# Performance work log

Measured on AMD Instinct MI355X. Metric: run time of the kernel, lower is better.

Reference implementation:

```python
import jax, jax.numpy as jnp
import numpy as np

EPS = 1e-7
BURN_IN = 3
INNER_STEPS = 2
N_FEAT, N_TARGET, N_LATENT = 262144, 8192, 32


def setup_inputs() -> dict:
    key = jax.random.key(0)
    ks = jax.random.split(key, 8)
    x = jax.random.normal(ks[0], (N_FEAT,), jnp.float32)
    y = jax.random.normal(ks[1], (N_TARGET,), jnp.float32)
    mu_x = jnp.zeros((N_FEAT,), jnp.float32)
    mu_y = jnp.zeros((N_TARGET,), jnp.float32)
    u0 = jax.random.normal(ks[2], (N_LATENT,), jnp.float32)
    u = u0 / jnp.sqrt(jnp.sum(u0 ** 2))
    Wz = jax.random.normal(ks[3], (N_LATENT, N_FEAT), jnp.float32) * 0.1
    Cz = jax.random.normal(ks[4], (N_LATENT, N_TARGET), jnp.float32) * 0.1
    t_sq_sum = jax.random.uniform(ks[5], (N_LATENT,), jnp.float32) + 1.0
    bz = jax.random.normal(ks[6], (N_LATENT,), jnp.float32) * 0.1
    P = jax.random.normal(ks[7], (N_LATENT, N_FEAT), jnp.float32) * 0.1
    return dict(x=x, y=y, mu_x=mu_x, mu_y=mu_y, u=u, Wz=Wz, Cz=Cz,
                t_sq_sum=t_sq_sum, bz=bz, P=P, n=100)


def _partial_fit(x, y, mu_x, mu_y, u, Wz, Cz, t_sq_sum, bz, P, n):
    # n is a static Python int (sample count before this call)
    n_new = n + 1  # torch: self.n[:] = self.n + 1
    mu_x = (mu_x * n_new + x) / (n_new + 1)
    mu_y = (mu_y * n_new + y) / (n_new + 1)
    xc = x - mu_x
    yc = y - mu_y
    if n_new <= BURN_IN:
        # vectorized burn-in update; only Wz and t_sq_sum change
        Wz = Wz + xc[None, :] * u[:, None]
        tz = Wz @ xc / (jnp.sqrt(jnp.sum(Wz ** 2, axis=1)) + EPS)
        t_sq_sum = t_sq_sum + tz * tz
        return mu_x, mu_y, u, Wz, Cz, t_sq_sum, bz, P

    def comp_step(carry, comp):
        xr, yr = carry
        Wz_i, Cz_i, P_i, u_i, tss, bz_i = comp
        # inner power-iteration refinements (total INNER_STEPS passes)
        for _ in range(INNER_STEPS):
            wz = Wz_i + xr * u_i                                  # [n_feat]
            tz = xr @ wz / (jnp.sqrt(jnp.sum(wz ** 2)) + EPS)     # scalar
            tss_ = tss + tz * tz
            t = tz / jnp.sqrt(tss_)
            cz = Cz_i + yr * t                                    # [n_target]
            C_i = cz / jnp.sqrt(jnp.sum(cz ** 2))
            u_i = yr @ C_i
        bz_new = bz_i + u_i * tz
        b = bz_new / jnp.sqrt(tss_)
        P_new = P_i + xr * t
        xr2 = xr - t * P_new  # deflate x
        yr2 = yr - b * t * C_i  # deflate y
        return (xr2, yr2), (wz, cz, P_new, u_i, tss_, bz_new)

    (_, _), (Wz_n, Cz_n, P_n, u_n, tss_n, bz_n) = jax.lax.scan(
        comp_step, (xc, yc), (Wz, Cz, P, u, t_sq_sum, bz))
    return mu_x, mu_y, u_n, Wz_n, Cz_n, tss_n, bz_n, P_n


def reference(x, y, mu_x, mu_y, u, Wz, Cz, t_sq_sum, bz, P, n):
    outs = _partial_fit(x, y, mu_x, mu_y, u, Wz, Cz, t_sq_sum, bz, P, n)
    # concatenate updated state (mu_x, mu_y, u, Wz, Cz, t_sq_sum, bz, P)
    return jnp.concatenate([o.ravel() for o in outs])
```

## Files before the change

kernel.cpp:

```cpp
#include <hip/hip_runtime.h>


#define NF 262144
#define NT 8192
#define NL 32
#define GYS 36
#define LDSW 260

#define NBX 1024
#define KS  256
#define CHK 128
#define NSLOT 512
#define GXW 68
#define PBE 2276
#define DIAG 2244

#define WS_PART 0
#define WS_GY   (NSLOT*PBE)
#define WS_GX   (WS_GY + GYS*GYS)
#define WS_CNT  (WS_GX + PBE)
#define WS_COEF (WS_CNT + 4)

#define OUT_MU_X 0
#define OUT_MU_Y 262144
#define OUT_U    270336
#define OUT_WZ   270368
#define OUT_CZ   8658976
#define OUT_TSS  8921120
#define OUT_BZ   8921152
#define OUT_P    8921184

typedef __attribute__((ext_vector_type(8))) short bf16x8;
typedef __attribute__((ext_vector_type(4))) float f32x4;

__device__ __forceinline__ float4 ld4(const float* p) { return *(const float4*)p; }

__device__ __forceinline__ unsigned int f2bf_rne(float f) {
  unsigned int t = __float_as_uint(f);
  t += 0x7FFFu + ((t >> 16) & 1u);
  return t >> 16;
}

__device__ __forceinline__ double rsq64(double x) {
  double r = __builtin_amdgcn_rsq(x);
  r = r * (1.5 - 0.5 * x * r * r);
  return r;
}

__global__ __launch_bounds__(320) void gram_kernel(
    const float* __restrict__ x, const float* __restrict__ y,
    const float* __restrict__ mux, const float* __restrict__ muy,
    const float* __restrict__ Wz, const float* __restrict__ Cz,
    const float* __restrict__ P, const int* __restrict__ np,
    float* __restrict__ ws)
{
  __shared__ __align__(16) char smem[80 * CHK * 4 + 128];
  const int tid = threadIdx.x;
  const int b = blockIdx.x;
  const float n1 = (float)(np[0] + 1);
  const float cmu = n1 / (n1 + 1.0f);

  if (b < NBX) {
    char* hB = smem;
    char* lB = smem + 80 * CHK * 2;
    float* PB = ws + WS_PART + (size_t)(b & (NSLOT - 1)) * PBE;

    {
      unsigned int* hz = (unsigned int*)hB;
      unsigned int* lz = (unsigned int*)lB;
      for (int i = tid; i < 960; i += 320) { hz[65 * 64 + i] = 0u; lz[65 * 64 + i] = 0u; }
    }

    f32x4 acc0 = {0.f, 0.f, 0.f, 0.f};
    f32x4 acc1 = acc0, acc2 = acc0;
    const int lane = tid & 63;
    const int w = tid >> 6;
    const int col16 = lane & 15;
    const int kgrp = lane >> 4;
    const int swz = (col16 & 7) << 4;

    float4 v[7]; float4 vm0;

    auto issue = [&](int c) {
      const int kb = b * KS + c * CHK;
#pragma unroll
      for (int it = 0; it < 7; ++it) {
        int idx = tid + it * 320;
        if (idx < 2080) {
          int row = idx >> 5;
          int c4 = idx & 31;
          int k = kb + c4 * 4;
          const float* bp = (row == 0) ? (x + k)
                          : (row < 33) ? (P + (size_t)(row - 1) * NF + k)
                                       : (Wz + (size_t)(row - 33) * NF + k);
          v[it] = ld4(bp);
          if (it == 0 && row == 0) vm0 = ld4(mux + k);
        }
      }
    };

    auto convert_write = [&]() {
#pragma unroll
      for (int it = 0; it < 7; ++it) {
        int idx = tid + it * 320;
        if (idx < 2080) {
          int row = idx >> 5;
          int c4 = idx & 31;
          float4 t4 = v[it];
          if (it == 0 && row == 0) {
            t4.x = cmu * (t4.x - vm0.x); t4.y = cmu * (t4.y - vm0.y);
            t4.z = cmu * (t4.z - vm0.z); t4.w = cmu * (t4.w - vm0.w);
          }
          if (row >= 33) {
            float sq = t4.x * t4.x + t4.y * t4.y + t4.z * t4.z + t4.w * t4.w;
            sq += __shfl_xor(sq, 1, 64);
            sq += __shfl_xor(sq, 2, 64);
            sq += __shfl_xor(sq, 4, 64);
            sq += __shfl_xor(sq, 8, 64);
            sq += __shfl_xor(sq, 16, 64);
            if ((tid & 31) == 0) atomicAdd(&PB[DIAG + row - 33], sq);
          }
          unsigned int b0 = __float_as_uint(t4.x), b1 = __float_as_uint(t4.y);
          unsigned int b2 = __float_as_uint(t4.z), b3 = __float_as_uint(t4.w);
          float h0 = __uint_as_float(b0 & 0xFFFF0000u);
          float h1 = __uint_as_float(b1 & 0xFFFF0000u);
          float h2 = __uint_as_float(b2 & 0xFFFF0000u);
          float h3 = __uint_as_float(b3 & 0xFFFF0000u);
          uint2 hw, lw;
          hw.x = (b0 >> 16) | ((b1 >> 16) << 16);
          hw.y = (b2 >> 16) | ((b3 >> 16) << 16);
          lw.x = f2bf_rne(t4.x - h0) | (f2bf_rne(t4.y - h1) << 16);
          lw.y = f2bf_rne(t4.z - h2) | (f2bf_rne(t4.w - h3) << 16);
          int off = ((row << 8) + (c4 << 3)) ^ ((row & 7) << 4);
          *(uint2*)(hB + off) = hw;
          *(uint2*)(lB + off) = lw;
        }
      }
    };

    auto compute_chunk = [&]() {
#pragma unroll
      for (int s = 0; s < 4; ++s) {
        const int kbyte = s * 64 + kgrp * 16;
        const int oa = ((col16 << 8) + kbyte) ^ swz;
        const int ob = oa + (w << 12);
        bf16x8 bh = *(const bf16x8*)(hB + ob);
        bf16x8 bl = *(const bf16x8*)(lB + ob);
        bf16x8 a0h = *(const bf16x8*)(hB + oa);
        bf16x8 a0l = *(const bf16x8*)(lB + oa);
        acc0 = __builtin_amdgcn_mfma_f32_16x16x32_bf16(a0h, bh, acc0, 0, 0, 0);
        acc0 = __builtin_amdgcn_mfma_f32_16x16x32_bf16(a0h, bl, acc0, 0, 0, 0);
        acc0 = __builtin_amdgcn_mfma_f32_16x16x32_bf16(a0l, bh, acc0, 0, 0, 0);
        acc0 = __builtin_amdgcn_mfma_f32_16x16x32_bf16(a0l, bl, acc0, 0, 0, 0);
        bf16x8 a1h = *(const bf16x8*)(hB + oa + 4096);
        bf16x8 a1l = *(const bf16x8*)(lB + oa + 4096);
        acc1 = __builtin_amdgcn_mfma_f32_16x16x32_bf16(a1h, bh, acc1, 0, 0, 0);
        acc1 = __builtin_amdgcn_mfma_f32_16x16x32_bf16(a1h, bl, acc1, 0, 0, 0);
        acc1 = __builtin_amdgcn_mfma_f32_16x16x32_bf16(a1l, bh, acc1, 0, 0, 0);
        acc1 = __builtin_amdgcn_mfma_f32_16x16x32_bf16(a1l, bl, acc1, 0, 0, 0);
        bf16x8 a2h = *(const bf16x8*)(hB + oa + 8192);
        bf16x8 a2l = *(const bf16x8*)(lB + oa + 8192);
        acc2 = __builtin_amdgcn_mfma_f32_16x16x32_bf16(a2h, bh, acc2, 0, 0, 0);
        acc2 = __builtin_amdgcn_mfma_f32_16x16x32_bf16(a2h, bl, acc2, 0, 0, 0);
        acc2 = __builtin_amdgcn_mfma_f32_16x16x32_bf16(a2l, bh, acc2, 0, 0, 0);
        acc2 = __builtin_amdgcn_mfma_f32_16x16x32_bf16(a2l, bl, acc2, 0, 0, 0);
      }
    };

    issue(0);
    convert_write();
    __syncthreads();
    issue(1);
    compute_chunk();
    __syncthreads();
    convert_write();
    __syncthreads();
    compute_chunk();

    const int vcol = w * 16 + col16;
    if (vcol < 65) {
#pragma unroll
      for (int r2 = 0; r2 < 4; ++r2) {
        int u = kgrp * 4 + r2;
        atomicAdd(&PB[u * GXW + vcol], acc0[r2]);
        atomicAdd(&PB[(16 + u) * GXW + vcol], acc1[r2]);
      }
      if (kgrp == 0) atomicAdd(&PB[32 * GXW + vcol], acc2[0]);
    }
  } else {
    float* lds = (float*)smem;
    float* GY = ws + WS_GY;
    const int yb = b - NBX;
    int gu = 0, gv = 0; bool active = (tid < 45);
    if (active) {
      int pp = tid;
      for (int g = 0; g < 9; ++g) {
        int cnt = 9 - g;
        if (pp < cnt) { gu = g; gv = g + pp; break; }
        pp -= cnt;
      }
    }
    float acc[16];
#pragma unroll
    for (int i = 0; i < 16; ++i) acc[i] = 0.f;
    const int wb = yb * 256;
    float4 vy[8]; float4 vmy;
#pragma unroll
    for (int it = 0; it < 8; ++it) {
      int idx = tid + it * 320;
      if (idx < 2304) {
        int row = idx >> 6;
        int c4 = idx & 63;
        int k = wb + c4 * 4;
        if (row == 0) {
          vy[it] = ld4(y + k);
          if (it == 0) vmy = ld4(muy + k);
        } else if (row < 33) {
          vy[it] = ld4(Cz + (size_t)(row - 1) * NT + k);
        } else {
          vy[it] = make_float4(0.f, 0.f, 0.f, 0.f);
        }
      }
    }
#pragma unroll
    for (int it = 0; it < 8; ++it) {
      int idx = tid + it * 320;
      if (idx < 2304) {
        int row = idx >> 6;
        int c4 = idx & 63;
        float4 t4 = vy[it];
        if (it == 0 && row == 0) {
          t4.x = cmu * (t4.x - vmy.x); t4.y = cmu * (t4.y - vmy.y);
          t4.z = cmu * (t4.z - vmy.z); t4.w = cmu * (t4.w - vmy.w);
        }
        *(float4*)&lds[row * LDSW + c4 * 4] = t4;
      }
    }
    __syncthreads();
    if (active) {
      const int ub = 4 * gu * LDSW, vb = 4 * gv * LDSW;
      for (int c = 0; c < 64; ++c) {
        float4 av[4], bv[4];
#pragma unroll
        for (int r = 0; r < 4; ++r) av[r] = *(const float4*)&lds[ub + r * LDSW + c * 4];
#pragma unroll
        for (int s = 0; s < 4; ++s) bv[s] = *(const float4*)&lds[vb + s * LDSW + c * 4];
#pragma unroll
        for (int r = 0; r < 4; ++r)
#pragma unroll
          for (int s = 0; s < 4; ++s)
            acc[r * 4 + s] += av[r].x * bv[s].x + av[r].y * bv[s].y +
                              av[r].z * bv[s].z + av[r].w * bv[s].w;
      }
#pragma unroll
      for (int r = 0; r < 4; ++r)
#pragma unroll
        for (int s = 0; s < 4; ++s) {
          int u = 4 * gu + r, v = 4 * gv + s;
          if (u < 33 && v < 33) {
            float val = acc[r * 4 + s];
            atomicAdd(&GY[u * GYS + v], val);
            if (gu != gv) atomicAdd(&GY[v * GYS + u], val);
          }
        }
    }
  }
}

__device__ __forceinline__ void solve_body(
    const float* __restrict__ ws, const float* __restrict__ u_in,
    const float* __restrict__ tss_in, const float* __restrict__ bz_in,
    float* __restrict__ coef, float* __restrict__ out)
{
  const int l = threadIdx.x;
  const float* GX = ws + WS_GX;
  const float* GY = ws + WS_GY;
  float* AWZT = coef;
  float* APT  = coef + 33 * NL;
  float* ACZT = coef + 66 * NL;

  float rP[32], rW[32], rC[32];
#pragma unroll
  for (int i = 0; i < 32; ++i) rP[i] = GX[(1 + i) * GXW + 1 + l];
#pragma unroll
  for (int i = 0; i < 32; ++i) rW[i] = (l < 32) ? GX[(1 + i) * GXW + 33 + l] : 0.f;
#pragma unroll
  for (int i = 0; i < 32; ++i) rC[i] = GY[(1 + i) * GYS + 1 + l];
  float dS  = (l < 32) ? GX[DIAG + l] : 0.f;
  float u0l = (l < 32) ? u_in[l]   : 0.f;
  float t0l = (l < 32) ? tss_in[l] : 0.f;
  float b0l = (l < 32) ? bz_in[l]  : 0.f;

  double q = (double)GX[0];
  double r = (double)GY[0];
  double pj = (l < 32) ? (double)GX[1 + l]  : 0.0;
  double wj = (l < 32) ? (double)GX[33 + l] : 0.0;
  double ej = (l < 32) ? (double)GY[1 + l]  : 0.0;
  double cx = (l == 0) ? 1.0 : 0.0;
  double cy = (l == 0) ? 1.0 : 0.0;

#pragma unroll
  for (int i = 0; i < NL; ++i) {
    double a  = __shfl(wj, i, 64);
    double g  = __shfl(ej, i, 64);
    double pi = __shfl(pj, i, 64);
    double s  = (double)__shfl(dS, i, 64);
    double h  = (double)__shfl(rC[i], i, 64);
    double Pd = (double)__shfl(rP[i], i, 64);
    double u0   = (double)__shfl(u0l, i, 64);
    double tss0 = (double)__shfl(t0l, i, 64);
    double bz0  = (double)__shfl(b0l, i, 64);

    double ui = u0, u1 = 0.0, tz = 0.0, tss_ = 0.0, t = 0.0;
    double rt = 0.0, rn = 0.0;
#pragma unroll
    for (int pass = 0; pass < 2; ++pass) {
      double num = a + ui * q;
      double s2  = s + 2.0 * ui * a + ui * ui * q;
      double rs  = rsq64(s2);
      tz = num * rs * (1.0 - 1e-7 * rs);
      tss_ = tss0 + tz * tz;
      rt = rsq64(tss_);
      t  = tz * rt;
      double ncz2 = h + 2.0 * t * g + t * t * r;
      rn = rsq64(ncz2);
      ui = (g + t * r) * rn;
      if (pass == 0) u1 = ui;
    }
    double u2 = ui;
    double bz_new = bz0 + u2 * tz;
    double bb = bz_new * rt;
    double phi = 1.0 - t * t;
    double gam = bb * t * rn;
    double psi = 1.0 - gam * t;

    if (l == 0) {
      out[OUT_U + i]   = (float)u2;
      out[OUT_TSS + i] = (float)tss_;
      out[OUT_BZ + i]  = (float)bz_new;
    }
    if (l < 33) {
      AWZT[l * 32 + i] = (float)(u1 * cx);
      APT [l * 32 + i] = (float)(t  * cx) + ((l == 1 + i) ? 1.0f : 0.0f);
      ACZT[l * 32 + i] = (float)(t  * cy) + ((l == 1 + i) ? 1.0f : 0.0f);
    }
    q = phi * phi * q - 2.0 * phi * t * pi + t * t * Pd;
    r = psi * psi * r - 2.0 * psi * gam * g + gam * gam * h;
    cx *= phi; if (l == 1 + i) cx -= t;
    cy *= psi; if (l == 1 + i) cy -= gam;
    if (l < 32) {
      pj = phi * pj - t * (double)rP[i];
      wj = phi * wj - t * (double)rW[i];
      ej = psi * ej - gam * (double)rC[i];
    }
  }
}

__global__ __launch_bounds__(256) void redsolve_kernel(
    float* __restrict__ ws, const float* __restrict__ u_in,
    const float* __restrict__ tss_in, const float* __restrict__ bz_in,
    float* __restrict__ coef, float* __restrict__ out)
{
  const int e = (blockIdx.x % 9) * 256 + threadIdx.x;
  const int c = blockIdx.x / 9;
  if (e < PBE) {
    const float* PB = ws + WS_PART + (size_t)(c * 64) * PBE + e;
    float s0 = 0.f, s1 = 0.f, s2 = 0.f, s3 = 0.f;
#pragma unroll
    for (int j = 0; j < 64; j += 4) {
      s0 += PB[(size_t)j * PBE];
      s1 += PB[(size_t)(j + 1) * PBE];
      s2 += PB[(size_t)(j + 2) * PBE];
      s3 += PB[(size_t)(j + 3) * PBE];
    }
    atomicAdd(ws + WS_GX + e, (s0 + s1) + (s2 + s3));
  }
  __threadfence();
  __shared__ int lastflag;
  if (threadIdx.x == 0) {
    int old = atomicAdd((int*)(ws + WS_CNT), 1);
    lastflag = (old == 71);
  }
  __syncthreads();
  if (!lastflag) return;
  __threadfence();
  if (threadIdx.x < 64) solve_body(ws, u_in, tss_in, bz_in, coef, out);
}

__global__ __launch_bounds__(256) void out_kernel(
    const float* __restrict__ x, const float* __restrict__ y,
    const float* __restrict__ mux, const float* __restrict__ muy,
    const float* __restrict__ Wz, const float* __restrict__ Cz,
    const float* __restrict__ P, const int* __restrict__ np,
    const float* __restrict__ coef, float* __restrict__ out)
{
  const int b = blockIdx.x, tid = threadIdx.x;
  const float n1 = (float)(np[0] + 1);
  const float inv = 1.0f / (n1 + 1.0f);
  const float* AWZT = coef;
  const float* APT  = coef + 33 * NL;
  const float* ACZT = coef + 66 * NL;

  if (b < 1024) {
    const int k = b * 256 + tid;
    float xv = x[k], mv = mux[k];
    float mn = (mv * n1 + xv) * inv;
    out[OUT_MU_X + k] = mn;
    float accW[32], accP[32];
#pragma unroll
    for (int i = 0; i < 32; ++i) accW[i] = Wz[(size_t)i * NF + k];
#pragma unroll
    for (int i = 0; i < 32; ++i) accP[i] = 0.f;
    {
      float B0 = xv - mn;
#pragma unroll
      for (int i = 0; i < 32; ++i) {
        accW[i] += AWZT[i] * B0;
        accP[i] += APT[i] * B0;
      }
    }
#pragma unroll 4
    for (int j = 1; j < 33; ++j) {
      float Bj = P[(size_t)(j - 1) * NF + k];
      const float* cw = AWZT + j * 32;
      const float* cp = APT + j * 32;
#pragma unroll
      for (int i = 0; i < 32; ++i) {
        accW[i] += cw[i] * Bj;
        accP[i] += cp[i] * Bj;
      }
    }
#pragma unroll
    for (int i = 0; i < 32; ++i) out[OUT_WZ + (size_t)i * NF + k] = accW[i];
#pragma unroll
    for (int i = 0; i < 32; ++i) out[OUT_P + (size_t)i * NF + k] = accP[i];
  } else {
    const int k = (b - 1024) * 256 + tid;
    float yv = y[k], mv = muy[k];
    float mn = (mv * n1 + yv) * inv;
    out[OUT_MU_Y + k] = mn;
    float accC[32];
#pragma unroll
    for (int i = 0; i < 32; ++i) accC[i] = 0.f;
    {
      float B0 = yv - mn;
#pragma unroll
      for (int i = 0; i < 32; ++i) accC[i] += ACZT[i] * B0;
    }
#pragma unroll 4
    for (int j = 1; j < 33; ++j) {
      float Bj = Cz[(size_t)(j - 1) * NT + k];
      const float* cc = ACZT + j * 32;
#pragma unroll
      for (int i = 0; i < 32; ++i) accC[i] += cc[i] * Bj;
    }
#pragma unroll
    for (int i = 0; i < 32; ++i) out[OUT_CZ + (size_t)i * NT + k] = accC[i];
  }
}

extern "C" void kernel_launch(void* const* d_in, const int* in_sizes, int n_in,
                              void* d_out, int out_size, void* d_ws, size_t ws_size,
                              hipStream_t stream) {
  const float* x   = (const float*)d_in[0];
  const float* y   = (const float*)d_in[1];
  const float* mux = (const float*)d_in[2];
  const float* muy = (const float*)d_in[3];
  const float* u   = (const float*)d_in[4];
  const float* Wz  = (const float*)d_in[5];
  const float* Cz  = (const float*)d_in[6];
  const float* tss = (const float*)d_in[7];
  const float* bz  = (const float*)d_in[8];
  const float* P   = (const float*)d_in[9];
  const int*   n   = (const int*)d_in[10];
  float* ws  = (float*)d_ws;
  float* out = (float*)d_out;

  hipMemsetAsync(ws, 0, (size_t)(NSLOT * PBE + GYS * GYS + PBE + 4) * sizeof(float), stream);
  gram_kernel<<<NBX + 32, 320, 0, stream>>>(x, y, mux, muy, Wz, Cz, P, n, ws);
  redsolve_kernel<<<72, 256, 0, stream>>>(ws, u, tss, bz, ws + WS_COEF, out);
  out_kernel<<<1024 + 32, 256, 0, stream>>>(x, y, mux, muy, Wz, Cz, P, n, ws + WS_COEF, out);
}
```

Before: 220.4 us.

## Give each Gram block its own partial slot and loop over eight smaller chunks

Measured after the change: 208.7 us. -5.3%, faster.

```diff
diff --git a/kernel.cpp b/kernel.cpp
--- a/kernel.cpp
+++ b/kernel.cpp
@@ -5,18 +5,19 @@
 #define NT 8192
 #define NL 32
 #define GYS 36
-#define LDSW 260
-
-#define NBX 1024
-#define KS  256
-#define CHK 128
-#define NSLOT 512
+#define LDSWY 132
+
+#define NBX 512
+#define NBY 64
+#define KS  512
+#define CHK 64
+#define NCHK 8
 #define GXW 68
 #define PBE 2276
 #define DIAG 2244
 
 #define WS_PART 0
-#define WS_GY   (NSLOT*PBE)
+#define WS_GY   (NBX*PBE)
 #define WS_GX   (WS_GY + GYS*GYS)
 #define WS_CNT  (WS_GX + PBE)
 #define WS_COEF (WS_CNT + 4)
@@ -54,7 +55,7 @@
     const float* __restrict__ P, const int* __restrict__ np,
     float* __restrict__ ws)
 {
-  __shared__ __align__(16) char smem[80 * CHK * 4 + 128];
+  __shared__ __align__(16) char smem[20608];
   const int tid = threadIdx.x;
   const int b = blockIdx.x;
   const float n1 = (float)(np[0] + 1);
@@ -63,13 +64,16 @@
   if (b < NBX) {
     char* hB = smem;
     char* lB = smem + 80 * CHK * 2;
-    float* PB = ws + WS_PART + (size_t)(b & (NSLOT - 1)) * PBE;
-
+    float* sdiag = (float*)(smem + 80 * CHK * 4);
+    float* PB = ws + WS_PART + (size_t)b * PBE;
+
+    if (tid < 32) sdiag[tid] = 0.f;
     {
       unsigned int* hz = (unsigned int*)hB;
       unsigned int* lz = (unsigned int*)lB;
-      for (int i = tid; i < 960; i += 320) { hz[65 * 64 + i] = 0u; lz[65 * 64 + i] = 0u; }
-    }
+      for (int i = tid; i < 480; i += 320) { hz[2080 + i] = 0u; lz[2080 + i] = 0u; }
+    }
+    __syncthreads();
 
     f32x4 acc0 = {0.f, 0.f, 0.f, 0.f};
     f32x4 acc1 = acc0, acc2 = acc0;
@@ -79,16 +83,16 @@
     const int kgrp = lane >> 4;
     const int swz = (col16 & 7) << 4;
 
-    float4 v[7]; float4 vm0;
+    float4 v[4]; float4 vm0;
 
     auto issue = [&](int c) {
       const int kb = b * KS + c * CHK;
 #pragma unroll
-      for (int it = 0; it < 7; ++it) {
+      for (int it = 0; it < 4; ++it) {
         int idx = tid + it * 320;
-        if (idx < 2080) {
-          int row = idx >> 5;
-          int c4 = idx & 31;
+        if (idx < 1040) {
+          int row = idx >> 4;
+          int c4 = idx & 15;
           int k = kb + c4 * 4;
           const float* bp = (row == 0) ? (x + k)
                           : (row < 33) ? (P + (size_t)(row - 1) * NF + k)
@@ -101,11 +105,11 @@
 
     auto convert_write = [&]() {
 #pragma unroll
-      for (int it = 0; it < 7; ++it) {
+      for (int it = 0; it < 4; ++it) {
         int idx = tid + it * 320;
-        if (idx < 2080) {
-          int row = idx >> 5;
-          int c4 = idx & 31;
+        if (idx < 1040) {
+          int row = idx >> 4;
+          int c4 = idx & 15;
           float4 t4 = v[it];
           if (it == 0 && row == 0) {
             t4.x = cmu * (t4.x - vm0.x); t4.y = cmu * (t4.y - vm0.y);
@@ -117,8 +121,7 @@
             sq += __shfl_xor(sq, 2, 64);
             sq += __shfl_xor(sq, 4, 64);
             sq += __shfl_xor(sq, 8, 64);
-            sq += __shfl_xor(sq, 16, 64);
-            if ((tid & 31) == 0) atomicAdd(&PB[DIAG + row - 33], sq);
+            if ((tid & 15) == 0) atomicAdd(&sdiag[row - 33], sq);
           }
           unsigned int b0 = __float_as_uint(t4.x), b1 = __float_as_uint(t4.y);
           unsigned int b2 = __float_as_uint(t4.z), b3 = __float_as_uint(t4.w);
@@ -131,7 +134,7 @@
           hw.y = (b2 >> 16) | ((b3 >> 16) << 16);
           lw.x = f2bf_rne(t4.x - h0) | (f2bf_rne(t4.y - h1) << 16);
           lw.y = f2bf_rne(t4.z - h2) | (f2bf_rne(t4.w - h3) << 16);
-          int off = ((row << 8) + (c4 << 3)) ^ ((row & 7) << 4);
+          int off = ((row << 7) + (c4 << 3)) ^ ((row & 7) << 4);
           *(uint2*)(hB + off) = hw;
           *(uint2*)(lB + off) = lw;
         }
@@ -140,10 +143,10 @@
 
     auto compute_chunk = [&]() {
 #pragma unroll
-      for (int s = 0; s < 4; ++s) {
+      for (int s = 0; s < 2; ++s) {
         const int kbyte = s * 64 + kgrp * 16;
-        const int oa = ((col16 << 8) + kbyte) ^ swz;
-        const int ob = oa + (w << 12);
+        const int oa = ((col16 << 7) + kbyte) ^ swz;
+        const int ob = oa + (w << 11);
         bf16x8 bh = *(const bf16x8*)(hB + ob);
         bf16x8 bl = *(const bf16x8*)(lB + ob);
         bf16x8 a0h = *(const bf16x8*)(hB + oa);
@@ -152,14 +155,14 @@
         acc0 = __builtin_amdgcn_mfma_f32_16x16x32_bf16(a0h, bl, acc0, 0, 0, 0);
         acc0 = __builtin_amdgcn_mfma_f32_16x16x32_bf16(a0l, bh, acc0, 0, 0, 0);
         acc0 = __builtin_amdgcn_mfma_f32_16x16x32_bf16(a0l, bl, acc0, 0, 0, 0);
-        bf16x8 a1h = *(const bf16x8*)(hB + oa + 4096);
-        bf16x8 a1l = *(const bf16x8*)(lB + oa + 4096);
+        bf16x8 a1h = *(const bf16x8*)(hB + oa + 2048);
+        bf16x8 a1l = *(const bf16x8*)(lB + oa + 2048);
         acc1 = __builtin_amdgcn_mfma_f32_16x16x32_bf16(a1h, bh, acc1, 0, 0, 0);
         acc1 = __builtin_amdgcn_mfma_f32_16x16x32_bf16(a1h, bl, acc1, 0, 0, 0);
         acc1 = __builtin_amdgcn_mfma_f32_16x16x32_bf16(a1l, bh, acc1, 0, 0, 0);
         acc1 = __builtin_amdgcn_mfma_f32_16x16x32_bf16(a1l, bl, acc1, 0, 0, 0);
-        bf16x8 a2h = *(const bf16x8*)(hB + oa + 8192);
-        bf16x8 a2l = *(const bf16x8*)(lB + oa + 8192);
+        bf16x8 a2h = *(const bf16x8*)(hB + oa + 4096);
+        bf16x8 a2l = *(const bf16x8*)(lB + oa + 4096);
         acc2 = __builtin_amdgcn_mfma_f32_16x16x32_bf16(a2h, bh, acc2, 0, 0, 0);
         acc2 = __builtin_amdgcn_mfma_f32_16x16x32_bf16(a2h, bl, acc2, 0, 0, 0);
         acc2 = __builtin_amdgcn_mfma_f32_16x16x32_bf16(a2l, bh, acc2, 0, 0, 0);
@@ -172,21 +175,25 @@
     __syncthreads();
     issue(1);
     compute_chunk();
-    __syncthreads();
-    convert_write();
-    __syncthreads();
-    compute_chunk();
+    for (int c = 1; c < NCHK; ++c) {
+      __syncthreads();
+      convert_write();
+      __syncthreads();
+      if (c + 1 < NCHK) issue(c + 1);
+      compute_chunk();
+    }
 
     const int vcol = w * 16 + col16;
     if (vcol < 65) {
 #pragma unroll
       for (int r2 = 0; r2 < 4; ++r2) {
         int u = kgrp * 4 + r2;
-        atomicAdd(&PB[u * GXW + vcol], acc0[r2]);
-        atomicAdd(&PB[(16 + u) * GXW + vcol], acc1[r2]);
-      }
-      if (kgrp == 0) atomicAdd(&PB[32 * GXW + vcol], acc2[0]);
-    }
+        PB[u * GXW + vcol] = acc0[r2];
+        PB[(16 + u) * GXW + vcol] = acc1[r2];
+      }
+      if (kgrp == 0) PB[32 * GXW + vcol] = acc2[0];
+    }
+    if (tid < 32) PB[DIAG + tid] = sdiag[tid];
   } else {
     float* lds = (float*)smem;
     float* GY = ws + WS_GY;
@@ -203,14 +210,14 @@
     float acc[16];
 #pragma unroll
     for (int i = 0; i < 16; ++i) acc[i] = 0.f;
-    const int wb = yb * 256;
-    float4 vy[8]; float4 vmy;
-#pragma unroll
-    for (int it = 0; it < 8; ++it) {
+    const int wb = yb * 128;
+    float4 vy[4]; float4 vmy;
+#pragma unroll
+    for (int it = 0; it < 4; ++it) {
       int idx = tid + it * 320;
-      if (idx < 2304) {
-        int row = idx >> 6;
-        int c4 = idx & 63;
+      if (idx < 1152) {
+        int row = idx >> 5;
+        int c4 = idx & 31;
         int k = wb + c4 * 4;
         if (row == 0) {
           vy[it] = ld4(y + k);
@@ -223,28 +230,28 @@
       }
     }
 #pragma unroll
-    for (int it = 0; it < 8; ++it) {
+    for (int it = 0; it < 4; ++it) {
       int idx = tid + it * 320;
-      if (idx < 2304) {
-        int row = idx >> 6;
-        int c4 = idx & 63;
+      if (idx < 1152) {
+        int row = idx >> 5;
+        int c4 = idx & 31;
         float4 t4 = vy[it];
         if (it == 0 && row == 0) {
           t4.x = cmu * (t4.x - vmy.x); t4.y = cmu * (t4.y - vmy.y);
           t4.z = cmu * (t4.z - vmy.z); t4.w = cmu * (t4.w - vmy.w);
         }
-        *(float4*)&lds[row * LDSW + c4 * 4] = t4;
+        *(float4*)&lds[row * LDSWY + c4 * 4] = t4;
       }
     }
     __syncthreads();
     if (active) {
-      const int ub = 4 * gu * LDSW, vb = 4 * gv * LDSW;
-      for (int c = 0; c < 64; ++c) {
+      const int ub = 4 * gu * LDSWY, vb = 4 * gv * LDSWY;
+      for (int c = 0; c < 32; ++c) {
         float4 av[4], bv[4];
 #pragma unroll
-        for (int r = 0; r < 4; ++r) av[r] = *(const float4*)&lds[ub + r * LDSW + c * 4];
-#pragma unroll
-        for (int s = 0; s < 4; ++s) bv[s] = *(const float4*)&lds[vb + s * LDSW + c * 4];
+        for (int r = 0; r < 4; ++r) av[r] = *(const float4*)&lds[ub + r * LDSWY + c * 4];
+#pragma unroll
+        for (int s = 0; s < 4; ++s) bv[s] = *(const float4*)&lds[vb + s * LDSWY + c * 4];
 #pragma unroll
         for (int r = 0; r < 4; ++r)
 #pragma unroll
@@ -419,7 +426,7 @@
         accP[i] += APT[i] * B0;
       }
     }
-#pragma unroll 4
+#pragma unroll 8
     for (int j = 1; j < 33; ++j) {
       float Bj = P[(size_t)(j - 1) * NF + k];
       const float* cw = AWZT + j * 32;
@@ -447,7 +454,7 @@
 #pragma unroll
       for (int i = 0; i < 32; ++i) accC[i] += ACZT[i] * B0;
     }
-#pragma unroll 4
+#pragma unroll 8
     for (int j = 1; j < 33; ++j) {
       float Bj = Cz[(size_t)(j - 1) * NT + k];
       const float* cc = ACZT + j * 32;
@@ -476,8 +483,8 @@
   float* ws  = (float*)d_ws;
   float* out = (float*)d_out;
 
-  hipMemsetAsync(ws, 0, (size_t)(NSLOT * PBE + GYS * GYS + PBE + 4) * sizeof(float), stream);
-  gram_kernel<<<NBX + 32, 320, 0, stream>>>(x, y, mux, muy, Wz, Cz, P, n, ws);
+  hipMemsetAsync(ws + WS_GY, 0, (size_t)(GYS * GYS + PBE + 4) * sizeof(float), stream);
+  gram_kernel<<<NBX + NBY, 320, 0, stream>>>(x, y, mux, muy, Wz, Cz, P, n, ws);
   redsolve_kernel<<<72, 256, 0, stream>>>(ws, u, tss, bz, ws + WS_COEF, out);
   out_kernel<<<1024 + 32, 256, 0, stream>>>(x, y, mux, muy, Wz, Cz, P, n, ws + WS_COEF, out);
 }
```
